# Kernel tuning notes

Measured on AMD Instinct MI355X. Metric: run time of the kernel, lower is better.

## Reference

```python
import jax, jax.numpy as jnp
import numpy as np

N_NODES = 50000
N_EDGES = 1250000
D = 64


def setup_inputs() -> dict:
    key = jax.random.key(0)
    ks = jax.random.split(key, 9)
    s = 1.0 / np.sqrt(D)
    return {
        "y": jax.random.normal(ks[0], (N_NODES, D), dtype=jnp.float32),
        "src": jax.random.randint(ks[1], (N_EDGES,), 0, N_NODES, dtype=jnp.int32),
        "dst": jax.random.randint(ks[2], (N_EDGES,), 0, N_NODES, dtype=jnp.int32),
        "W1": jax.random.normal(ks[3], (D, D), dtype=jnp.float32) * s,
        "b1": jnp.zeros((D,), dtype=jnp.float32),
        "W2": jax.random.normal(ks[4], (D, D), dtype=jnp.float32) * s,
        "b2": jnp.zeros((D,), dtype=jnp.float32),
        "U1": jax.random.normal(ks[5], (D, D), dtype=jnp.float32) * s,
        "c1": jnp.zeros((D,), dtype=jnp.float32),
        "U2": jax.random.normal(ks[6], (D, D), dtype=jnp.float32) * s,
        "c2": jnp.zeros((D,), dtype=jnp.float32),
    }


def reference(y, src, dst, W1, b1, W2, b2, U1, c1, U2, c2):
    # msg = relu(FNN_pre(y[src])) ; FNN = Linear -> ReLU -> Linear
    xs = y[src]                                        # [E, D] gather
    h1 = jax.nn.relu(xs @ W1 + b1)                     # [E, D]
    msg = jax.nn.relu(h1 @ W2 + b2)                    # [E, D]
    # z = segment-sum of messages at destination nodes
    z = jax.ops.segment_sum(msg, dst, num_segments=N_NODES)  # [N, D]
    # h = relu(FNN_update(z))
    h2 = jax.nn.relu(z @ U1 + c1)                      # [N, D]
    h = jax.nn.relu(h2 @ U2 + c2)                      # [N, D]
    return h
```

## Files before the change

kernel.cpp:

```cpp
#include <hip/hip_runtime.h>

#define D 64
#define CHUNK 4096
#define BSHIFT 8
#define MAXB 8192

typedef unsigned int uint;
typedef unsigned short ushort;

using bf16x8 = __attribute__((ext_vector_type(8))) short;
using f32x4  = __attribute__((ext_vector_type(4))) float;

__device__ __forceinline__ uint f2bf(float f) {
    uint u = __float_as_uint(f);
    return (u + 0x7fffu + ((u >> 16) & 1u)) >> 16;
}
__device__ __forceinline__ uint pk2(float a, float b) {
    return f2bf(a) | (f2bf(b) << 16);
}

#define ACC8M(v, aE, aO, mk) do {                                              \
    aE[0] = fmaf(mk, __uint_as_float((v).x << 16), aE[0]);                     \
    aO[0] = fmaf(mk, __uint_as_float((v).x & 0xffff0000u), aO[0]);             \
    aE[1] = fmaf(mk, __uint_as_float((v).y << 16), aE[1]);                     \
    aO[1] = fmaf(mk, __uint_as_float((v).y & 0xffff0000u), aO[1]);             \
    aE[2] = fmaf(mk, __uint_as_float((v).z << 16), aE[2]);                     \
    aO[2] = fmaf(mk, __uint_as_float((v).z & 0xffff0000u), aO[2]);             \
    aE[3] = fmaf(mk, __uint_as_float((v).w << 16), aE[3]);                     \
    aO[3] = fmaf(mk, __uint_as_float((v).w & 0xffff0000u), aO[3]);             \
} while (0)

template <bool BF16IN, bool BF16OUT>
__device__ __forceinline__ void mlp_tile(
    int tile, ushort (*Hs)[72],
    const float* __restrict__ Xf, const ushort* __restrict__ Xb,
    const float* __restrict__ W1, const float* __restrict__ b1v,
    const float* __restrict__ W2, const float* __restrict__ b2v,
    ushort* __restrict__ out16, float* __restrict__ out32, int N)
{
    const int lane = threadIdx.x & 63;
    const int m = lane & 15;
    const int q = lane >> 4;

    bf16x8 w1f[4][2], w2f[4][2];
    #pragma unroll
    for (int t = 0; t < 4; ++t) {
        const int n = t * 16 + m;
        #pragma unroll
        for (int kf = 0; kf < 2; ++kf) {
            bf16x8 f1, f2;
            #pragma unroll
            for (int j = 0; j < 8; ++j) {
                const int k = kf * 32 + q * 8 + j;
                f1[j] = (short)f2bf(W1[k * D + n]);
                f2[j] = (short)f2bf(W2[k * D + n]);
            }
            w1f[t][kf] = f1;
            w2f[t][kf] = f2;
        }
    }

    const int rowbase = tile * 16;
    int r = rowbase + m;
    if (r >= N) r = N - 1;
    bf16x8 ax0, ax1;
    if (BF16IN) {
        const ushort* xr = Xb + (size_t)r * D + q * 8;
        ax0 = *(const bf16x8*)xr;
        ax1 = *(const bf16x8*)(xr + 32);
    } else {
        const float* xr = Xf + (size_t)r * D + q * 8;
        float4 x0 = *(const float4*)xr;
        float4 x1 = *(const float4*)(xr + 4);
        float4 x2 = *(const float4*)(xr + 32);
        float4 x3 = *(const float4*)(xr + 36);
        ax0[0]=(short)f2bf(x0.x); ax0[1]=(short)f2bf(x0.y);
        ax0[2]=(short)f2bf(x0.z); ax0[3]=(short)f2bf(x0.w);
        ax0[4]=(short)f2bf(x1.x); ax0[5]=(short)f2bf(x1.y);
        ax0[6]=(short)f2bf(x1.z); ax0[7]=(short)f2bf(x1.w);
        ax1[0]=(short)f2bf(x2.x); ax1[1]=(short)f2bf(x2.y);
        ax1[2]=(short)f2bf(x2.z); ax1[3]=(short)f2bf(x2.w);
        ax1[4]=(short)f2bf(x3.x); ax1[5]=(short)f2bf(x3.y);
        ax1[6]=(short)f2bf(x3.z); ax1[7]=(short)f2bf(x3.w);
    }

    const f32x4 zero4 = {0.f, 0.f, 0.f, 0.f};
    f32x4 acc[4];

    #pragma unroll
    for (int t = 0; t < 4; ++t) acc[t] = zero4;
    #pragma unroll
    for (int t = 0; t < 4; ++t) {
        acc[t] = __builtin_amdgcn_mfma_f32_16x16x32_bf16(ax0, w1f[t][0], acc[t], 0, 0, 0);
        acc[t] = __builtin_amdgcn_mfma_f32_16x16x32_bf16(ax1, w1f[t][1], acc[t], 0, 0, 0);
    }
    #pragma unroll
    for (int t = 0; t < 4; ++t) {
        const float bv = b1v[t * 16 + m];
        #pragma unroll
        for (int rg = 0; rg < 4; ++rg) {
            float hv = fmaxf(acc[t][rg] + bv, 0.f);
            Hs[q * 4 + rg][t * 16 + m] = (ushort)f2bf(hv);
        }
    }
    __syncthreads();

    bf16x8 ah0 = *(const bf16x8*)&Hs[m][q * 8];
    bf16x8 ah1 = *(const bf16x8*)&Hs[m][32 + q * 8];

    #pragma unroll
    for (int t = 0; t < 4; ++t) acc[t] = zero4;
    #pragma unroll
    for (int t = 0; t < 4; ++t) {
        acc[t] = __builtin_amdgcn_mfma_f32_16x16x32_bf16(ah0, w2f[t][0], acc[t], 0, 0, 0);
        acc[t] = __builtin_amdgcn_mfma_f32_16x16x32_bf16(ah1, w2f[t][1], acc[t], 0, 0, 0);
    }
    #pragma unroll
    for (int t = 0; t < 4; ++t) {
        const float bv = b2v[t * 16 + m];
        #pragma unroll
        for (int rg = 0; rg < 4; ++rg) {
            const int row = rowbase + q * 4 + rg;
            if (row < N) {
                float ov = fmaxf(acc[t][rg] + bv, 0.f);
                if (BF16OUT) out16[(size_t)row * D + t * 16 + m] = (ushort)f2bf(ov);
                else         out32[(size_t)row * D + t * 16 + m] = ov;
            }
        }
    }
}

__global__ __launch_bounds__(256) void kA_mlp_hist(
    const float* __restrict__ y,
    const float* __restrict__ W1, const float* __restrict__ b1,
    const float* __restrict__ W2, const float* __restrict__ b2,
    ushort* __restrict__ msg16, int N,
    const int* __restrict__ dst, int* __restrict__ histG, int E, int NBA)
{
    __shared__ __align__(16) ushort Hs[4][16][72];
    __shared__ int lhist[256];
    const int t = threadIdx.x;
    if ((int)blockIdx.x < NBA) {
        lhist[t] = 0;
        __syncthreads();
        const int cbase = blockIdx.x * CHUNK;
        const int lim = min(CHUNK, E - cbase);
        if (lim == CHUNK) {
            const int4* dp = (const int4*)(dst + cbase);
            int4 d4[4];
            #pragma unroll
            for (int g = 0; g < 4; ++g) d4[g] = dp[g * 256 + t];
            #pragma unroll
            for (int g = 0; g < 4; ++g) {
                atomicAdd(&lhist[(uint)d4[g].x >> BSHIFT], 1);
                atomicAdd(&lhist[(uint)d4[g].y >> BSHIFT], 1);
                atomicAdd(&lhist[(uint)d4[g].z >> BSHIFT], 1);
                atomicAdd(&lhist[(uint)d4[g].w >> BSHIFT], 1);
            }
        } else {
            for (int j = t; j < lim; j += 256)
                atomicAdd(&lhist[(uint)dst[cbase + j] >> BSHIFT], 1);
        }
        __syncthreads();
        histG[blockIdx.x * 256 + t] = lhist[t];
    } else {
        const int tile = (blockIdx.x - NBA) * 4 + (t >> 6);
        mlp_tile<false, true>(tile, Hs[t >> 6], y, nullptr, W1, b1, W2, b2,
                              msg16, nullptr, N);
    }
}

__global__ __launch_bounds__(256) void kB_scan(
    const int* __restrict__ histG, int* __restrict__ startG,
    int* __restrict__ tot, int NBA)
{
    __shared__ int tmp[256];
    const int t = threadIdx.x;
    const int b = blockIdx.x;
    const int i0 = 2 * t, i1 = 2 * t + 1;
    int v0 = (i0 < NBA) ? histG[i0 * 256 + b] : 0;
    int v1 = (i1 < NBA) ? histG[i1 * 256 + b] : 0;
    int s = v0 + v1;
    int x = s; tmp[t] = x; __syncthreads();
    #pragma unroll
    for (int off = 1; off < 256; off <<= 1) {
        int add = (t >= off) ? tmp[t - off] : 0; __syncthreads();
        x += add; tmp[t] = x; __syncthreads();
    }
    int excl = x - s;
    if (i0 < NBA) startG[i0 * 256 + b] = excl;
    if (i1 < NBA) startG[i1 * 256 + b] = excl + v0;
    if (t == 255) tot[b] = x;
}

__global__ __launch_bounds__(256) void kC_partition(
    const int* __restrict__ src, const int* __restrict__ dst,
    const int* __restrict__ startG, const int* __restrict__ tot,
    uint* __restrict__ packedG, int E)
{
    __shared__ int t1[256];
    __shared__ int cur[256];
    const int t = threadIdx.x;
    int tv = tot[t];
    int x = tv; t1[t] = x; __syncthreads();
    #pragma unroll
    for (int off = 1; off < 256; off <<= 1) {
        int add = (t >= off) ? t1[t - off] : 0; __syncthreads();
        x += add; t1[t] = x; __syncthreads();
    }
    cur[t] = (x - tv) + startG[blockIdx.x * 256 + t];
    __syncthreads();
    const int cbase = blockIdx.x * CHUNK;
    const int lim = min(CHUNK, E - cbase);
    if (lim == CHUNK) {
        const int4* sp = (const int4*)(src + cbase);
        const int4* dp = (const int4*)(dst + cbase);
        int4 s4[4], d4[4];
        #pragma unroll
        for (int g = 0; g < 4; ++g) { s4[g] = sp[g * 256 + t]; d4[g] = dp[g * 256 + t]; }
        #pragma unroll
        for (int g = 0; g < 4; ++g) {
            int pos;
            pos = atomicAdd(&cur[(uint)d4[g].x >> BSHIFT], 1);
            packedG[pos] = ((uint)(d4[g].x & 255) << 16) | (uint)s4[g].x;
            pos = atomicAdd(&cur[(uint)d4[g].y >> BSHIFT], 1);
            packedG[pos] = ((uint)(d4[g].y & 255) << 16) | (uint)s4[g].y;
            pos = atomicAdd(&cur[(uint)d4[g].z >> BSHIFT], 1);
            packedG[pos] = ((uint)(d4[g].z & 255) << 16) | (uint)s4[g].z;
            pos = atomicAdd(&cur[(uint)d4[g].w >> BSHIFT], 1);
            packedG[pos] = ((uint)(d4[g].w & 255) << 16) | (uint)s4[g].w;
        }
    } else {
        for (int j = t; j < lim; j += 256) {
            const int e = cbase + j;
            int s = src[e], d = dst[e];
            int pos = atomicAdd(&cur[(uint)d >> BSHIFT], 1);
            packedG[pos] = ((uint)(d & 255) << 16) | (uint)s;
        }
    }
}

__global__ __launch_bounds__(256) void kF_place(
    const uint* __restrict__ packedG, const int* __restrict__ tot,
    ushort* __restrict__ sortedG, int* __restrict__ offsets, int N, int E)
{
    __shared__ int t1[256];
    __shared__ int cnt[256];
    __shared__ int cur[256];
    __shared__ uint pk[MAXB];
    __shared__ ushort srt[MAXB];
    const int t = threadIdx.x;
    const int b = blockIdx.x;

    int tv = tot[t];
    int x = tv; t1[t] = x; __syncthreads();
    #pragma unroll
    for (int off = 1; off < 256; off <<= 1) {
        int add = (t >= off) ? t1[t - off] : 0; __syncthreads();
        x += add; t1[t] = x; __syncthreads();
    }
    const int pbase = (b == 0) ? 0 : t1[b - 1];
    const int cn = tot[b];
    const bool fits = (cn <= MAXB);

    cnt[t] = 0;
    __syncthreads();
    if (fits) {
        for (int i = t; i < cn; i += 256) pk[i] = packedG[pbase + i];
        __syncthreads();
        for (int i = t; i < cn; i += 256) atomicAdd(&cnt[pk[i] >> 16], 1);
    } else {
        for (int i = t; i < cn; i += 256)
            atomicAdd(&cnt[packedG[pbase + i] >> 16], 1);
    }
    __syncthreads();

    int c = cnt[t];
    int x2 = c; t1[t] = x2; __syncthreads();
    #pragma unroll
    for (int off = 1; off < 256; off <<= 1) {
        int add = (t >= off) ? t1[t - off] : 0; __syncthreads();
        x2 += add; t1[t] = x2; __syncthreads();
    }
    const int excl = x2 - c;
    const int node = b * 256 + t;
    if (node < N) offsets[node] = pbase + excl;
    if (b == 0 && t == 0) offsets[N] = E;

    if (fits) {
        cur[t] = excl;
        __syncthreads();
        for (int i = t; i < cn; i += 256) {
            uint e = pk[i];
            int p = atomicAdd(&cur[e >> 16], 1);
            srt[p] = (ushort)(e & 0xffffu);
        }
        __syncthreads();
        for (int i = t; i < cn; i += 256)
            sortedG[pbase + i] = srt[i];
    } else {
        cur[t] = pbase + excl;
        __syncthreads();
        for (int i = t; i < cn; i += 256) {
            uint e = packedG[pbase + i];
            int p = atomicAdd(&cur[e >> 16], 1);
            sortedG[p] = (ushort)(e & 0xffffu);
        }
    }
}

__global__ __launch_bounds__(256, 6) void k5_gather(
    const ushort* __restrict__ msg16,
    const int* __restrict__ offsets, const ushort* __restrict__ sortedG,
    ushort* __restrict__ z16, int n_nodes)
{
    const int lane = threadIdx.x & 63;
    const int sub = lane & 7;
    const int grp = (lane >> 3) & 3;
    const int half = lane >> 5;
    const int p = blockIdx.x * 4 + (threadIdx.x >> 6);
    if (p * 2 >= n_nodes) return;
    const ushort* mbase = msg16 + (sub << 3);

    const int n = 2 * p + half;
    const bool nvalid = n < n_nodes;
    int beg = 0, end = 0;
    if (nvalid) { beg = offsets[n]; end = offsets[n + 1]; }
    const int m = end - beg;
    const int m0 = __builtin_amdgcn_readfirstlane(m);
    const int m1 = __builtin_amdgcn_readlane(m, 32);
    const int mmax = max(m0, m1);

    float aE[4] = {0, 0, 0, 0}, aO[4] = {0, 0, 0, 0};

    for (int base = 0; base < mmax; base += 32) {
        int s[8];
        float mk[8];
        #pragma unroll
        for (int j = 0; j < 8; ++j) {
            if (base + j * 4 < mmax) {
                const int e = base + j * 4 + grp;
                const bool on = (e < m);
                mk[j] = on ? 1.f : 0.f;
                s[j] = (int)sortedG[on ? (beg + e) : 0];
            }
        }
        uint4 v[8];
        #pragma unroll
        for (int j = 0; j < 8; ++j)
            if (base + j * 4 < mmax)
                v[j] = *(const uint4*)(mbase + ((size_t)s[j] << 6));
        #pragma unroll
        for (int j = 0; j < 8; ++j)
            if (base + j * 4 < mmax) { ACC8M(v[j], aE, aO, mk[j]); }
    }

    #pragma unroll
    for (int d2 = 0; d2 < 4; ++d2) {
        aE[d2] += __shfl_xor(aE[d2], 8, 64);
        aO[d2] += __shfl_xor(aO[d2], 8, 64);
        aE[d2] += __shfl_xor(aE[d2], 16, 64);
        aO[d2] += __shfl_xor(aO[d2], 16, 64);
    }
    if (grp == 0 && nvalid) {
        uint4 pv;
        pv.x = pk2(aE[0], aO[0]);
        pv.y = pk2(aE[1], aO[1]);
        pv.z = pk2(aE[2], aO[2]);
        pv.w = pk2(aE[3], aO[3]);
        *(uint4*)(z16 + (size_t)n * D + (sub << 3)) = pv;
    }
}

__global__ __launch_bounds__(256) void k_mlp2(
    const ushort* __restrict__ z16,
    const float* __restrict__ U1, const float* __restrict__ c1,
    const float* __restrict__ U2, const float* __restrict__ c2,
    float* __restrict__ out, int N)
{
    __shared__ __align__(16) ushort Hs[4][16][72];
    const int tile = blockIdx.x * 4 + (threadIdx.x >> 6);
    mlp_tile<true, false>(tile, Hs[threadIdx.x >> 6], nullptr, z16,
                          U1, c1, U2, c2, nullptr, out, N);
}

extern "C" void kernel_launch(void* const* d_in, const int* in_sizes, int n_in,
                              void* d_out, int out_size, void* d_ws, size_t ws_size,
                              hipStream_t stream) {
    const float* y  = (const float*)d_in[0];
    const int*  src = (const int*) d_in[1];
    const int*  dst = (const int*) d_in[2];
    const float* W1 = (const float*)d_in[3];
    const float* b1 = (const float*)d_in[4];
    const float* W2 = (const float*)d_in[5];
    const float* b2 = (const float*)d_in[6];
    const float* U1 = (const float*)d_in[7];
    const float* c1 = (const float*)d_in[8];
    const float* U2 = (const float*)d_in[9];
    const float* c2 = (const float*)d_in[10];

    const int N = in_sizes[0] / D;
    const int E = in_sizes[1];
    const int NBA   = (E + CHUNK - 1) / CHUNK;
    const int NBUCK = (N + 255) / 256;
    const int NT    = (N + 15) / 16;
    const int MB    = (NT + 3) / 4;
    const int G5    = (N / 2 + 3) / 4;

    char* ws = (char*)d_ws;
    auto al16 = [](size_t x) { return (x + 15) & ~15ull; };
    ushort* msg16   = (ushort*)ws;  ws += al16((size_t)N * D * 2);
    int*    offsets = (int*)ws;     ws += al16((size_t)(N + 1) * 4);
    int*    tot     = (int*)ws;     ws += al16(256 * 4);
    ushort* sortedG = (ushort*)ws;  ws += al16((size_t)E * 2);
    ushort* z16     = (ushort*)ws;
    int*    histG   = (int*)ws;
    int*    startG  = histG + (size_t)NBA * 256;
    uint*   packedG = (uint*)(startG + (size_t)NBA * 256);

    kA_mlp_hist<<<NBA + MB, 256, 0, stream>>>(
        y, W1, b1, W2, b2, msg16, N, dst, histG, E, NBA);

    kB_scan<<<256, 256, 0, stream>>>(histG, startG, tot, NBA);

    kC_partition<<<NBA, 256, 0, stream>>>(src, dst, startG, tot, packedG, E);

    kF_place<<<NBUCK, 256, 0, stream>>>(packedG, tot, sortedG, offsets, N, E);

    k5_gather<<<G5, 256, 0, stream>>>(msg16, offsets, sortedG, z16, N);

    k_mlp2<<<MB, 256, 0, stream>>>(z16, U1, c1, U2, c2, (float*)d_out, N);
}
```

Baseline: 149.1 us.

## Prepack weights into MFMA bf16 fragment layout and move MLP1 into partition kernel

A small set of blocks in the histogram kernel converts all four weight matrices into bf16 MFMA fragment order once, so every MLP tile loads its weights with a few vector loads. Before, each wave did strided scalar fp32 loads and converted them itself. The first edge MLP moves from the histogram kernel into the partition kernel, which changes how work is balanced across the stages. The scan kernel is generalized so each thread handles K chunks, making it valid for larger NBA. This adds a 32 KB workspace buffer and makes the MLP depend on the pack kernel having completed.

```diff
diff --git a/kernel.cpp b/kernel.cpp
--- a/kernel.cpp
+++ b/kernel.cpp
@@ -34,8 +34,8 @@
 __device__ __forceinline__ void mlp_tile(
     int tile, ushort (*Hs)[72],
     const float* __restrict__ Xf, const ushort* __restrict__ Xb,
-    const float* __restrict__ W1, const float* __restrict__ b1v,
-    const float* __restrict__ W2, const float* __restrict__ b2v,
+    const ushort* __restrict__ pkW1, const float* __restrict__ b1v,
+    const ushort* __restrict__ pkW2, const float* __restrict__ b2v,
     ushort* __restrict__ out16, float* __restrict__ out32, int N)
 {
     const int lane = threadIdx.x & 63;
@@ -45,18 +45,11 @@
     bf16x8 w1f[4][2], w2f[4][2];
     #pragma unroll
     for (int t = 0; t < 4; ++t) {
-        const int n = t * 16 + m;
         #pragma unroll
         for (int kf = 0; kf < 2; ++kf) {
-            bf16x8 f1, f2;
-            #pragma unroll
-            for (int j = 0; j < 8; ++j) {
-                const int k = kf * 32 + q * 8 + j;
-                f1[j] = (short)f2bf(W1[k * D + n]);
-                f2[j] = (short)f2bf(W2[k * D + n]);
-            }
-            w1f[t][kf] = f1;
-            w2f[t][kf] = f2;
+            const int off = ((t * 2 + kf) * 64 + lane) << 3;
+            w1f[t][kf] = *(const bf16x8*)(pkW1 + off);
+            w2f[t][kf] = *(const bf16x8*)(pkW2 + off);
         }
     }
 
@@ -130,14 +123,12 @@
     }
 }
 
-__global__ __launch_bounds__(256) void kA_mlp_hist(
-    const float* __restrict__ y,
-    const float* __restrict__ W1, const float* __restrict__ b1,
-    const float* __restrict__ W2, const float* __restrict__ b2,
-    ushort* __restrict__ msg16, int N,
-    const int* __restrict__ dst, int* __restrict__ histG, int E, int NBA)
-{
-    __shared__ __align__(16) ushort Hs[4][16][72];
+__global__ __launch_bounds__(256) void kA_hist_pack(
+    const int* __restrict__ dst, int* __restrict__ histG, int E, int NBA,
+    const float* __restrict__ W1, const float* __restrict__ W2,
+    const float* __restrict__ U1, const float* __restrict__ U2,
+    ushort* __restrict__ pkAll)
+{
     __shared__ int lhist[256];
     const int t = threadIdx.x;
     if ((int)blockIdx.x < NBA) {
@@ -164,9 +155,25 @@
         __syncthreads();
         histG[blockIdx.x * 256 + t] = lhist[t];
     } else {
-        const int tile = (blockIdx.x - NBA) * 4 + (t >> 6);
-        mlp_tile<false, true>(tile, Hs[t >> 6], y, nullptr, W1, b1, W2, b2,
-                              msg16, nullptr, N);
+        const int mtx = blockIdx.x - NBA;
+        const float* W = (mtx == 0) ? W1 : (mtx == 1) ? W2 : (mtx == 2) ? U1 : U2;
+        ushort* pk = pkAll + mtx * 4096;
+        for (int u = t; u < 512; u += 256) {
+            const int t_ = u >> 7;
+            const int rem = u & 127;
+            const int kf = rem >> 6;
+            const int lane = rem & 63;
+            const int q = lane >> 4, m = lane & 15;
+            const int n = t_ * 16 + m;
+            uint w[4];
+            #pragma unroll
+            for (int j2 = 0; j2 < 4; ++j2) {
+                const int k = kf * 32 + q * 8 + 2 * j2;
+                w[j2] = pk2(W[k * D + n], W[(k + 1) * D + n]);
+            }
+            uint4 v = { w[0], w[1], w[2], w[3] };
+            *(uint4*)(pk + (u << 3)) = v;
+        }
     }
 }
 
@@ -177,66 +184,90 @@
     __shared__ int tmp[256];
     const int t = threadIdx.x;
     const int b = blockIdx.x;
-    const int i0 = 2 * t, i1 = 2 * t + 1;
-    int v0 = (i0 < NBA) ? histG[i0 * 256 + b] : 0;
-    int v1 = (i1 < NBA) ? histG[i1 * 256 + b] : 0;
-    int s = v0 + v1;
+    const int K = (NBA + 255) / 256;
+    const int c0 = t * K;
+    int loc[8];
+    int s = 0;
+    #pragma unroll
+    for (int i = 0; i < 8; ++i) {
+        if (i < K) {
+            const int c = c0 + i;
+            loc[i] = s;
+            s += (c < NBA) ? histG[c * 256 + b] : 0;
+        }
+    }
     int x = s; tmp[t] = x; __syncthreads();
     #pragma unroll
     for (int off = 1; off < 256; off <<= 1) {
         int add = (t >= off) ? tmp[t - off] : 0; __syncthreads();
         x += add; tmp[t] = x; __syncthreads();
     }
-    int excl = x - s;
-    if (i0 < NBA) startG[i0 * 256 + b] = excl;
-    if (i1 < NBA) startG[i1 * 256 + b] = excl + v0;
+    const int base = x - s;
+    #pragma unroll
+    for (int i = 0; i < 8; ++i) {
+        if (i < K) {
+            const int c = c0 + i;
+            if (c < NBA) startG[c * 256 + b] = base + loc[i];
+        }
+    }
     if (t == 255) tot[b] = x;
 }
 
-__global__ __launch_bounds__(256) void kC_partition(
+__global__ __launch_bounds__(256) void kC_part_mlp1(
     const int* __restrict__ src, const int* __restrict__ dst,
     const int* __restrict__ startG, const int* __restrict__ tot,
-    uint* __restrict__ packedG, int E)
+    uint* __restrict__ packedG, int E, int NBA,
+    const float* __restrict__ y, const ushort* __restrict__ pkAll,
+    const float* __restrict__ b1, const float* __restrict__ b2,
+    ushort* __restrict__ msg16, int N)
 {
     __shared__ int t1[256];
     __shared__ int cur[256];
+    __shared__ __align__(16) ushort Hs[4][16][72];
     const int t = threadIdx.x;
-    int tv = tot[t];
-    int x = tv; t1[t] = x; __syncthreads();
-    #pragma unroll
-    for (int off = 1; off < 256; off <<= 1) {
-        int add = (t >= off) ? t1[t - off] : 0; __syncthreads();
-        x += add; t1[t] = x; __syncthreads();
-    }
-    cur[t] = (x - tv) + startG[blockIdx.x * 256 + t];
-    __syncthreads();
-    const int cbase = blockIdx.x * CHUNK;
-    const int lim = min(CHUNK, E - cbase);
-    if (lim == CHUNK) {
-        const int4* sp = (const int4*)(src + cbase);
-        const int4* dp = (const int4*)(dst + cbase);
-        int4 s4[4], d4[4];
-        #pragma unroll
-        for (int g = 0; g < 4; ++g) { s4[g] = sp[g * 256 + t]; d4[g] = dp[g * 256 + t]; }
-        #pragma unroll
-        for (int g = 0; g < 4; ++g) {
-            int pos;
-            pos = atomicAdd(&cur[(uint)d4[g].x >> BSHIFT], 1);
-            packedG[pos] = ((uint)(d4[g].x & 255) << 16) | (uint)s4[g].x;
-            pos = atomicAdd(&cur[(uint)d4[g].y >> BSHIFT], 1);
-            packedG[pos] = ((uint)(d4[g].y & 255) << 16) | (uint)s4[g].y;
-            pos = atomicAdd(&cur[(uint)d4[g].z >> BSHIFT], 1);
-            packedG[pos] = ((uint)(d4[g].z & 255) << 16) | (uint)s4[g].z;
-            pos = atomicAdd(&cur[(uint)d4[g].w >> BSHIFT], 1);
-            packedG[pos] = ((uint)(d4[g].w & 255) << 16) | (uint)s4[g].w;
+    if ((int)blockIdx.x < NBA) {
+        int tv = tot[t];
+        int x = tv; t1[t] = x; __syncthreads();
+        #pragma unroll
+        for (int off = 1; off < 256; off <<= 1) {
+            int add = (t >= off) ? t1[t - off] : 0; __syncthreads();
+            x += add; t1[t] = x; __syncthreads();
+        }
+        cur[t] = (x - tv) + startG[blockIdx.x * 256 + t];
+        __syncthreads();
+        const int cbase = blockIdx.x * CHUNK;
+        const int lim = min(CHUNK, E - cbase);
+        if (lim == CHUNK) {
+            const int4* sp = (const int4*)(src + cbase);
+            const int4* dp = (const int4*)(dst + cbase);
+            int4 s4[4], d4[4];
+            #pragma unroll
+            for (int g = 0; g < 4; ++g) { s4[g] = sp[g * 256 + t]; d4[g] = dp[g * 256 + t]; }
+            #pragma unroll
+            for (int g = 0; g < 4; ++g) {
+                int pos;
+                pos = atomicAdd(&cur[(uint)d4[g].x >> BSHIFT], 1);
+                packedG[pos] = ((uint)(d4[g].x & 255) << 16) | (uint)s4[g].x;
+                pos = atomicAdd(&cur[(uint)d4[g].y >> BSHIFT], 1);
+                packedG[pos] = ((uint)(d4[g].y & 255) << 16) | (uint)s4[g].y;
+                pos = atomicAdd(&cur[(uint)d4[g].z >> BSHIFT], 1);
+                packedG[pos] = ((uint)(d4[g].z & 255) << 16) | (uint)s4[g].z;
+                pos = atomicAdd(&cur[(uint)d4[g].w >> BSHIFT], 1);
+                packedG[pos] = ((uint)(d4[g].w & 255) << 16) | (uint)s4[g].w;
+            }
+        } else {
+            for (int j = t; j < lim; j += 256) {
+                const int e = cbase + j;
+                int s = src[e], d = dst[e];
+                int pos = atomicAdd(&cur[(uint)d >> BSHIFT], 1);
+                packedG[pos] = ((uint)(d & 255) << 16) | (uint)s;
+            }
         }
     } else {
-        for (int j = t; j < lim; j += 256) {
-            const int e = cbase + j;
-            int s = src[e], d = dst[e];
-            int pos = atomicAdd(&cur[(uint)d >> BSHIFT], 1);
-            packedG[pos] = ((uint)(d & 255) << 16) | (uint)s;
-        }
+        const int tile = (blockIdx.x - NBA) * 4 + (t >> 6);
+        mlp_tile<false, true>(tile, Hs[t >> 6], y, nullptr,
+                              pkAll + 0 * 4096, b1, pkAll + 1 * 4096, b2,
+                              msg16, nullptr, N);
     }
 }
 
@@ -373,15 +404,15 @@
 }
 
 __global__ __launch_bounds__(256) void k_mlp2(
-    const ushort* __restrict__ z16,
-    const float* __restrict__ U1, const float* __restrict__ c1,
-    const float* __restrict__ U2, const float* __restrict__ c2,
+    const ushort* __restrict__ z16, const ushort* __restrict__ pkAll,
+    const float* __restrict__ c1, const float* __restrict__ c2,
     float* __restrict__ out, int N)
 {
     __shared__ __align__(16) ushort Hs[4][16][72];
     const int tile = blockIdx.x * 4 + (threadIdx.x >> 6);
     mlp_tile<true, false>(tile, Hs[threadIdx.x >> 6], nullptr, z16,
-                          U1, c1, U2, c2, nullptr, out, N);
+                          pkAll + 2 * 4096, c1, pkAll + 3 * 4096, c2,
+                          nullptr, out, N);
 }
 
 extern "C" void kernel_launch(void* const* d_in, const int* in_sizes, int n_in,
@@ -413,21 +444,24 @@
     int*    offsets = (int*)ws;     ws += al16((size_t)(N + 1) * 4);
     int*    tot     = (int*)ws;     ws += al16(256 * 4);
     ushort* sortedG = (ushort*)ws;  ws += al16((size_t)E * 2);
+    ushort* pkAll   = (ushort*)ws;  ws += al16(4 * 4096 * 2);
     ushort* z16     = (ushort*)ws;
     int*    histG   = (int*)ws;
     int*    startG  = histG + (size_t)NBA * 256;
     uint*   packedG = (uint*)(startG + (size_t)NBA * 256);
 
-    kA_mlp_hist<<<NBA + MB, 256, 0, stream>>>(
-        y, W1, b1, W2, b2, msg16, N, dst, histG, E, NBA);
-
-    kB_scan<<<256, 256, 0, stream>>>(histG, startG, tot, NBA);
-
-    kC_partition<<<NBA, 256, 0, stream>>>(src, dst, startG, tot, packedG, E);
+    kA_hist_pack<<<NBA + 4, 256, 0, stream>>>(
+        dst, histG, E, NBA, W1, W2, U1, U2, pkAll);
+
+    kB_scan<<<NBUCK > 256 ? NBUCK : 256, 256, 0, stream>>>(histG, startG, tot, NBA);
+
+    kC_part_mlp1<<<NBA + MB, 256, 0, stream>>>(
+        src, dst, startG, tot, packedG, E, NBA,
+        y, pkAll, b1, b2, msg16, N);
 
     kF_place<<<NBUCK, 256, 0, stream>>>(packedG, tot, sortedG, offsets, N, E);
 
     k5_gather<<<G5, 256, 0, stream>>>(msg16, offsets, sortedG, z16, N);
 
-    k_mlp2<<<MB, 256, 0, stream>>>(z16, U1, c1, U2, c2, (float*)d_out, N);
-}
+    k_mlp2<<<MB, 256, 0, stream>>>(z16, pkAll, c1, c2, (float*)d_out, N);
+}
```

After: 140.9 us. -5.5%, faster.
